# Optimization experiments

Measured on AMD Instinct MI355X. Metric: run time of the kernel, lower is better.

The kernel has to match this reference:

```python
import jax, jax.numpy as jnp
import numpy as np

H = 1024        # hidden_size
F = 4096        # intermediate_size
E = 8           # num_local_experts
TOP_K = 2       # num_experts_per_tok
B, S = 1, 2048


def setup_inputs() -> dict:
    key = jax.random.key(0)
    k0, k1, k2, k3 = jax.random.split(key, 4)
    hidden_states = jax.random.normal(k0, (B, S, H), dtype=jnp.float32)
    # torch nn.Linear weights: gate [E_out, in]; experts stacked on leading axis
    gate_w = jax.random.normal(k1, (E, H), dtype=jnp.float32) * 0.02
    gate_up_w = jax.random.normal(k2, (E, 2 * F, H), dtype=jnp.float32) * 0.02
    down_w = jax.random.normal(k3, (E, H, F), dtype=jnp.float32) * 0.02
    return {"hidden_states": hidden_states, "gate_w": gate_w,
            "gate_up_w": gate_up_w, "down_w": down_w}


def reference(hidden_states, gate_w, gate_up_w, down_w):
    b, s, h = hidden_states.shape
    x = hidden_states.reshape(-1, h)                      # [T, H]
    # router: softmax in float32, top-k, renormalize
    router_logits = x @ gate_w.T                          # [T, E]
    probs = jax.nn.softmax(router_logits.astype(jnp.float32), axis=-1)
    topw, sel = jax.lax.top_k(probs, TOP_K)               # [T, K]
    topw = topw / jnp.sum(topw, axis=-1, keepdims=True)
    topw = topw.astype(x.dtype)
    # combine weights [T, E]: zero for unselected experts -> same math as
    # the per-expert gather/scatter loop (full capacity, no dropped tokens)
    combine = jnp.sum(jax.nn.one_hot(sel, E, dtype=x.dtype) * topw[..., None], axis=1)
    # all experts on all tokens (dense-equivalent of masked dispatch)
    gu = jnp.einsum('th,efh->etf', x, gate_up_w)          # [E, T, 2F]
    gate, up = gu[..., :F], gu[..., F:]
    hact = up * jax.nn.gelu(gate, approximate=False)      # [E, T, F]
    expert_out = jnp.einsum('etf,ehf->eth', hact, down_w) # [E, T, H]
    out = jnp.einsum('eth,te->th', expert_out, combine)   # [T, H]
    return out.reshape(b, s, h)
```

## Files before the change

### kernel.cpp

```cpp
#include <hip/hip_runtime.h>

#define Hdim 1024
#define Fdim 4096
#define NE   8
#define NT   2048
#define MT_MAX 16
#define KSPLIT 2

typedef __attribute__((ext_vector_type(8))) short short8;
typedef __attribute__((ext_vector_type(4))) short short4v;
typedef __attribute__((ext_vector_type(4))) float f32x4;

__device__ __forceinline__ unsigned short bf16r(float f) {
  union { float fv; unsigned u; } v; v.fv = f;
  unsigned u = v.u;
  return (unsigned short)((u + 0x7FFFu + ((u >> 16) & 1u)) >> 16);
}

__device__ __forceinline__ void gl_lds16(const void* g, void* l) {
  __builtin_amdgcn_global_load_lds(
      (const __attribute__((address_space(1))) unsigned int*)g,
      (__attribute__((address_space(3))) unsigned int*)l, 16, 0, 0);
}

__global__ __launch_bounds__(256)
void k_cvt(const float* __restrict__ src, unsigned short* __restrict__ dst, int n4) {
  int stride = gridDim.x * 256;
  for (int i = blockIdx.x * 256 + threadIdx.x; i < n4; i += stride) {
    float4 v = *(const float4*)(src + (size_t)i * 4);
    short4v s;
    s.x = (short)bf16r(v.x); s.y = (short)bf16r(v.y);
    s.z = (short)bf16r(v.z); s.w = (short)bf16r(v.w);
    *(short4v*)(dst + (size_t)i * 4) = s;
  }
}

__global__ void k_router(const float* __restrict__ x, const float* __restrict__ gw,
                         int* __restrict__ counts, int* __restrict__ sel,
                         float* __restrict__ selw) {
  int wave = threadIdx.x >> 6;
  int l    = threadIdx.x & 63;
  int t    = blockIdx.x * 4 + wave;
  const float* xp = x + (size_t)t * Hdim;
  float acc[NE];
#pragma unroll
  for (int e = 0; e < NE; e++) acc[e] = 0.f;
  for (int h = l; h < Hdim; h += 64) {
    float xv = xp[h];
#pragma unroll
    for (int e = 0; e < NE; e++) acc[e] += xv * gw[e * Hdim + h];
  }
#pragma unroll
  for (int e = 0; e < NE; e++) {
    float v = acc[e];
#pragma unroll
    for (int off = 32; off > 0; off >>= 1) v += __shfl_down(v, off, 64);
    acc[e] = v;
  }
  if (l == 0) {
    int b0 = 0; float v0 = acc[0];
    for (int e = 1; e < NE; e++) if (acc[e] > v0) { v0 = acc[e]; b0 = e; }
    int b1 = -1; float v1 = -1e30f;
    for (int e = 0; e < NE; e++) if (e != b0 && acc[e] > v1) { v1 = acc[e]; b1 = e; }
    float w0 = 1.f / (1.f + expf(v1 - v0));
    atomicAdd(&counts[b0], 1);
    atomicAdd(&counts[b1], 1);
    sel[2 * t]     = b0;
    sel[2 * t + 1] = b1;
    selw[2 * t]     = w0;
    selw[2 * t + 1] = 1.f - w0;
  }
}

__global__ void k_scatter(const int* __restrict__ counts, const int* __restrict__ sel,
                          const float* __restrict__ selw, int* __restrict__ offsets,
                          int* __restrict__ rowids, float* __restrict__ pairw,
                          int* __restrict__ tok2slot) {
  __shared__ int soff[NE];
  __shared__ int scur[NE];
  if (threadIdx.x == 0) {
    int s = 0;
    for (int e = 0; e < NE; e++) { soff[e] = s; offsets[e] = s; s += counts[e]; scur[e] = 0; }
  }
  __syncthreads();
  for (int t = threadIdx.x; t < NT; t += blockDim.x) {
#pragma unroll
    for (int j = 0; j < 2; j++) {
      int e = sel[2 * t + j];
      int p = atomicAdd(&scur[e], 1);
      int slot = soff[e] + p;
      rowids[slot]        = t;
      pairw[slot]         = selw[2 * t + j];
      tok2slot[2 * t + j] = slot;
    }
  }
}

__global__ __launch_bounds__(256, 2)
void k_gate_up_bf(const unsigned short* __restrict__ xbf, const unsigned short* __restrict__ wbf,
                  const int* __restrict__ counts, const int* __restrict__ offsets,
                  const int* __restrict__ rowids, unsigned short* __restrict__ hact) {
  int e  = blockIdx.y >> 4;
  int mt = blockIdx.y & 15;
  int n  = counts[e];
  if (mt * 128 >= n) return;
  int base = offsets[e];
  int row0 = mt * 128;
  int f0   = blockIdx.x * 64;

  __shared__ __align__(16) unsigned short As[128][64];
  __shared__ __align__(16) unsigned short Bs[128][64];
  __shared__ int rid[128];

  int tid = threadIdx.x;
  if (tid < 128) {
    int r = row0 + tid;
    rid[tid] = (r < n) ? rowids[base + r] : rowids[base];
  }
  __syncthreads();

  int crow  = tid >> 3;
  int cphys = tid & 7;
  const unsigned short* sa[4];
  const unsigned short* sb[4];
#pragma unroll
  for (int p = 0; p < 4; p++) {
    int R = p * 32 + crow;
    int csrc = cphys ^ (R & 7);
    sa[p] = xbf + (size_t)rid[R] * Hdim + csrc * 8;
    int fr = (R < 64) ? (f0 + R) : (Fdim + f0 + (R - 64));
    sb[p] = wbf + ((size_t)e * 2 * Fdim + fr) * Hdim + csrc * 8;
  }
  int w = tid >> 6, lane = tid & 63;
  unsigned short* da[4];
  unsigned short* db[4];
#pragma unroll
  for (int p = 0; p < 4; p++) {
    da[p] = &As[0][0] + p * 2048 + w * 512;
    db[p] = &Bs[0][0] + p * 2048 + w * 512;
  }

  int wy = w >> 1, wx = w & 1;
  int lrow = lane & 15, cq = lane >> 4;
  f32x4 acc[4][4] = {};

  for (int k0 = 0; k0 < Hdim; k0 += 64) {
#pragma unroll
    for (int p = 0; p < 4; p++) gl_lds16(sa[p] + k0, da[p]);
#pragma unroll
    for (int p = 0; p < 4; p++) gl_lds16(sb[p] + k0, db[p]);
    __syncthreads();
#pragma unroll
    for (int ks = 0; ks < 2; ks++) {
      int soff = ((ks * 4 + cq) ^ (lrow & 7)) * 8;
      short8 a[4], b[4];
#pragma unroll
      for (int i = 0; i < 4; i++) a[i] = *(const short8*)&As[wy * 64 + i * 16 + lrow][soff];
      b[0] = *(const short8*)&Bs[wx * 32 + lrow][soff];
      b[1] = *(const short8*)&Bs[wx * 32 + 16 + lrow][soff];
      b[2] = *(const short8*)&Bs[64 + wx * 32 + lrow][soff];
      b[3] = *(const short8*)&Bs[64 + wx * 32 + 16 + lrow][soff];
#pragma unroll
      for (int i = 0; i < 4; i++)
#pragma unroll
        for (int j = 0; j < 4; j++)
          acc[i][j] = __builtin_amdgcn_mfma_f32_16x16x32_bf16(a[i], b[j], acc[i][j], 0, 0, 0);
    }
    __syncthreads();
  }

  int quad = lane >> 4;
#pragma unroll
  for (int i = 0; i < 4; i++) {
#pragma unroll
    for (int r = 0; r < 4; r++) {
      int rl = row0 + wy * 64 + i * 16 + quad * 4 + r;
      if (rl < n) {
        size_t rowoff = (size_t)(base + rl) * Fdim + f0 + wx * 32;
#pragma unroll
        for (int j = 0; j < 2; j++) {
          float g = acc[i][j][r];
          float u = acc[i][j + 2][r];
          float ge = 0.5f * g * (1.f + erff(g * 0.70710678118654752f));
          hact[rowoff + j * 16 + lrow] = bf16r(u * ge);
        }
      }
    }
  }
}

__global__ __launch_bounds__(256, 2)
void k_down_bf(const unsigned short* __restrict__ hact, const unsigned short* __restrict__ dbf,
               const int* __restrict__ counts, const int* __restrict__ offsets,
               const float* __restrict__ pairw, float* __restrict__ part) {
  int e  = blockIdx.y >> 4;
  int mt = blockIdx.y & 15;
  int n  = counts[e];
  if (mt * 128 >= n) return;
  int base = offsets[e];
  int row0 = mt * 128;
  int h0   = blockIdx.x * 128;
  const int KC = Fdim / KSPLIT;
  int kbeg = blockIdx.z * KC;
  int kend = kbeg + KC;

  __shared__ __align__(16) unsigned short As[128][64];
  __shared__ __align__(16) unsigned short Bs[128][64];

  int tid = threadIdx.x;
  int crow  = tid >> 3;
  int cphys = tid & 7;
  const unsigned short* sa[4];
  const unsigned short* sb[4];
#pragma unroll
  for (int p = 0; p < 4; p++) {
    int R = p * 32 + crow;
    int csrc = cphys ^ (R & 7);
    int slot = base + row0 + R;
    if (slot > NT * 2 - 1) slot = NT * 2 - 1;
    sa[p] = hact + (size_t)slot * Fdim + csrc * 8;
    sb[p] = dbf + ((size_t)e * Hdim + h0 + R) * Fdim + csrc * 8;
  }
  int w = tid >> 6, lane = tid & 63;
  unsigned short* da[4];
  unsigned short* db[4];
#pragma unroll
  for (int p = 0; p < 4; p++) {
    da[p] = &As[0][0] + p * 2048 + w * 512;
    db[p] = &Bs[0][0] + p * 2048 + w * 512;
  }

  int wy = w >> 1, wx = w & 1;
  int lrow = lane & 15, cq = lane >> 4;
  f32x4 acc[4][4] = {};

  for (int k0 = kbeg; k0 < kend; k0 += 64) {
#pragma unroll
    for (int p = 0; p < 4; p++) gl_lds16(sa[p] + k0, da[p]);
#pragma unroll
    for (int p = 0; p < 4; p++) gl_lds16(sb[p] + k0, db[p]);
    __syncthreads();
#pragma unroll
    for (int ks = 0; ks < 2; ks++) {
      int soff = ((ks * 4 + cq) ^ (lrow & 7)) * 8;
      short8 a[4], b[4];
#pragma unroll
      for (int i = 0; i < 4; i++) a[i] = *(const short8*)&As[wy * 64 + i * 16 + lrow][soff];
#pragma unroll
      for (int j = 0; j < 4; j++) b[j] = *(const short8*)&Bs[wx * 64 + j * 16 + lrow][soff];
#pragma unroll
      for (int i = 0; i < 4; i++)
#pragma unroll
        for (int j = 0; j < 4; j++)
          acc[i][j] = __builtin_amdgcn_mfma_f32_16x16x32_bf16(a[i], b[j], acc[i][j], 0, 0, 0);
    }
    __syncthreads();
  }

  int quad = lane >> 4;
#pragma unroll
  for (int i = 0; i < 4; i++) {
#pragma unroll
    for (int r = 0; r < 4; r++) {
      int rl = row0 + wy * 64 + i * 16 + quad * 4 + r;
      if (rl < n) {
        int slot = base + rl;
        float wv = pairw[slot];
        float* op = part + ((size_t)blockIdx.z * (NT * 2) + slot) * Hdim + h0 + wx * 64;
#pragma unroll
        for (int j = 0; j < 4; j++)
          op[j * 16 + lrow] = wv * acc[i][j][r];
      }
    }
  }
}

__global__ __launch_bounds__(256, 2)
void k_gate_up_v1(const float* __restrict__ x, const float* __restrict__ gup,
                  const int* __restrict__ counts, const int* __restrict__ offsets,
                  const int* __restrict__ rowids, unsigned short* __restrict__ hact) {
  int e  = blockIdx.y >> 4;
  int mt = blockIdx.y & 15;
  int n  = counts[e];
  if (mt * 128 >= n) return;
  int base = offsets[e];
  int row0 = mt * 128;
  int f0   = blockIdx.x * 64;

  __shared__ __align__(16) unsigned short As[128][40];
  __shared__ __align__(16) unsigned short Bs[128][40];
  __shared__ int rid[128];

  int tid = threadIdx.x;
  if (tid < 128) {
    int r = row0 + tid;
    rid[tid] = (r < n) ? rowids[base + r] : rowids[base];
  }
  __syncthreads();

  int kc   = (tid & 7) * 4;
  int trow = tid >> 3;
  const float* ap[4];
  const float* bp[4];
#pragma unroll
  for (int p = 0; p < 4; p++) {
    int ar = p * 32 + trow;
    ap[p] = x + (size_t)rid[ar] * Hdim + kc;
    int f = (ar < 64) ? (f0 + ar) : (Fdim + f0 + (ar - 64));
    bp[p] = gup + ((size_t)e * 2 * Fdim + f) * Hdim + kc;
  }

  int wave = tid >> 6, lane = tid & 63;
  int wy = wave >> 1, wx = wave & 1;
  int lrow = lane & 15, lk = (lane >> 4) * 8;
  f32x4 acc[4][4] = {};

  float4 ra[4], rb[4];
#pragma unroll
  for (int p = 0; p < 4; p++) { ra[p] = *(const float4*)(ap[p]); rb[p] = *(const float4*)(bp[p]); }

  for (int k0 = 0; k0 < Hdim; k0 += 32) {
    __syncthreads();
#pragma unroll
    for (int p = 0; p < 4; p++) {
      int ar = p * 32 + trow;
      short4v sa;
      sa.x = (short)bf16r(ra[p].x); sa.y = (short)bf16r(ra[p].y);
      sa.z = (short)bf16r(ra[p].z); sa.w = (short)bf16r(ra[p].w);
      *(short4v*)&As[ar][kc] = sa;
      short4v sbv;
      sbv.x = (short)bf16r(rb[p].x); sbv.y = (short)bf16r(rb[p].y);
      sbv.z = (short)bf16r(rb[p].z); sbv.w = (short)bf16r(rb[p].w);
      *(short4v*)&Bs[ar][kc] = sbv;
    }
    if (k0 + 32 < Hdim) {
#pragma unroll
      for (int p = 0; p < 4; p++) {
        ra[p] = *(const float4*)(ap[p] + k0 + 32);
        rb[p] = *(const float4*)(bp[p] + k0 + 32);
      }
    }
    __syncthreads();
    short8 a[4], b[4];
#pragma unroll
    for (int i = 0; i < 4; i++) a[i] = *(const short8*)&As[wy * 64 + i * 16 + lrow][lk];
    b[0] = *(const short8*)&Bs[wx * 32 + lrow][lk];
    b[1] = *(const short8*)&Bs[wx * 32 + 16 + lrow][lk];
    b[2] = *(const short8*)&Bs[64 + wx * 32 + lrow][lk];
    b[3] = *(const short8*)&Bs[64 + wx * 32 + 16 + lrow][lk];
#pragma unroll
    for (int i = 0; i < 4; i++)
#pragma unroll
      for (int j = 0; j < 4; j++)
        acc[i][j] = __builtin_amdgcn_mfma_f32_16x16x32_bf16(a[i], b[j], acc[i][j], 0, 0, 0);
  }

  int quad = lane >> 4;
#pragma unroll
  for (int i = 0; i < 4; i++) {
#pragma unroll
    for (int r = 0; r < 4; r++) {
      int rl = row0 + wy * 64 + i * 16 + quad * 4 + r;
      if (rl < n) {
        size_t rowoff = (size_t)(base + rl) * Fdim + f0 + wx * 32;
#pragma unroll
        for (int j = 0; j < 2; j++) {
          float g = acc[i][j][r];
          float u = acc[i][j + 2][r];
          float ge = 0.5f * g * (1.f + erff(g * 0.70710678118654752f));
          hact[rowoff + j * 16 + lrow] = bf16r(u * ge);
        }
      }
    }
  }
}

__global__ __launch_bounds__(256, 2)
void k_down_v1(const unsigned short* __restrict__ hact, const float* __restrict__ dw,
               const int* __restrict__ counts, const int* __restrict__ offsets,
               const float* __restrict__ pairw, float* __restrict__ part) {
  int e  = blockIdx.y >> 4;
  int mt = blockIdx.y & 15;
  int n  = counts[e];
  if (mt * 128 >= n) return;
  int base = offsets[e];
  int row0 = mt * 128;
  int h0   = blockIdx.x * 128;
  const int KC = Fdim / KSPLIT;
  int kbeg = blockIdx.z * KC;
  int kend = kbeg + KC;

  __shared__ __align__(16) unsigned short As[128][72];
  __shared__ __align__(16) unsigned short Bs[128][72];

  int tid = threadIdx.x;
  int wave = tid >> 6, lane = tid & 63;
  int wy = wave >> 1, wx = wave & 1;
  int lrow = lane & 15, lkq = (lane >> 4) * 8;

  const unsigned short* asrc[4];
#pragma unroll
  for (int p = 0; p < 4; p++) {
    int idx = p * 256 + tid;
    int row = idx >> 3, seg = idx & 7;
    int slot = base + row0 + row;
    if (slot > NT * 2 - 1) slot = NT * 2 - 1;
    asrc[p] = hact + (size_t)slot * Fdim + seg * 8;
  }
  const float* bsrc[8];
#pragma unroll
  for (int p = 0; p < 8; p++) {
    int idx = p * 256 + tid;
    int row = idx >> 4, seg = idx & 15;
    bsrc[p] = dw + ((size_t)e * Hdim + h0 + row) * Fdim + seg * 4;
  }

  int4   raw[4];
  float4 rbw[8];
#pragma unroll
  for (int p = 0; p < 4; p++) raw[p] = *(const int4*)(asrc[p] + kbeg);
#pragma unroll
  for (int p = 0; p < 8; p++) rbw[p] = *(const float4*)(bsrc[p] + kbeg);

  f32x4 acc[4][4] = {};
  for (int k0 = kbeg; k0 < kend; k0 += 64) {
    __syncthreads();
#pragma unroll
    for (int p = 0; p < 4; p++) {
      int idx = p * 256 + tid;
      int row = idx >> 3, seg = idx & 7;
      *(int4*)&As[row][seg * 8] = raw[p];
    }
#pragma unroll
    for (int p = 0; p < 8; p++) {
      int idx = p * 256 + tid;
      int row = idx >> 4, seg = idx & 15;
      short4v sbv;
      sbv.x = (short)bf16r(rbw[p].x); sbv.y = (short)bf16r(rbw[p].y);
      sbv.z = (short)bf16r(rbw[p].z); sbv.w = (short)bf16r(rbw[p].w);
      *(short4v*)&Bs[row][seg * 4] = sbv;
    }
    if (k0 + 64 < kend) {
#pragma unroll
      for (int p = 0; p < 4; p++) raw[p] = *(const int4*)(asrc[p] + k0 + 64);
#pragma unroll
      for (int p = 0; p < 8; p++) rbw[p] = *(const float4*)(bsrc[p] + k0 + 64);
    }
    __syncthreads();
#pragma unroll
    for (int ks = 0; ks < 2; ks++) {
      short8 a[4], b[4];
#pragma unroll
      for (int i = 0; i < 4; i++) a[i] = *(const short8*)&As[wy * 64 + i * 16 + lrow][ks * 32 + lkq];
#pragma unroll
      for (int j = 0; j < 4; j++) b[j] = *(const short8*)&Bs[wx * 64 + j * 16 + lrow][ks * 32 + lkq];
#pragma unroll
      for (int i = 0; i < 4; i++)
#pragma unroll
        for (int j = 0; j < 4; j++)
          acc[i][j] = __builtin_amdgcn_mfma_f32_16x16x32_bf16(a[i], b[j], acc[i][j], 0, 0, 0);
    }
  }

  int quad = lane >> 4;
#pragma unroll
  for (int i = 0; i < 4; i++) {
#pragma unroll
    for (int r = 0; r < 4; r++) {
      int rl = row0 + wy * 64 + i * 16 + quad * 4 + r;
      if (rl < n) {
        int slot = base + rl;
        float wv = pairw[slot];
        float* op = part + ((size_t)blockIdx.z * (NT * 2) + slot) * Hdim + h0 + wx * 64;
#pragma unroll
        for (int j = 0; j < 4; j++)
          op[j * 16 + lrow] = wv * acc[i][j][r];
      }
    }
  }
}

__global__ __launch_bounds__(256)
void k_combine(const float* __restrict__ part, const int* __restrict__ tok2slot,
               float* __restrict__ out) {
  int idx = blockIdx.x * 256 + threadIdx.x;
  int t  = idx >> 8;
  int hc = (idx & 255) << 2;
  int s0 = tok2slot[2 * t];
  int s1 = tok2slot[2 * t + 1];
  float4 a = *(const float4*)&part[(size_t)s0 * Hdim + hc];
  float4 b = *(const float4*)&part[((size_t)(NT * 2) + s0) * Hdim + hc];
  float4 c = *(const float4*)&part[(size_t)s1 * Hdim + hc];
  float4 d = *(const float4*)&part[((size_t)(NT * 2) + s1) * Hdim + hc];
  float4 s;
  s.x = (a.x + b.x) + (c.x + d.x);
  s.y = (a.y + b.y) + (c.y + d.y);
  s.z = (a.z + b.z) + (c.z + d.z);
  s.w = (a.w + b.w) + (c.w + d.w);
  *(float4*)&out[(size_t)t * Hdim + hc] = s;
}

extern "C" void kernel_launch(void* const* d_in, const int* in_sizes, int n_in,
                              void* d_out, int out_size, void* d_ws, size_t ws_size,
                              hipStream_t stream) {
  const float* x   = (const float*)d_in[0];
  const float* gw  = (const float*)d_in[1];
  const float* gup = (const float*)d_in[2];
  const float* dwn = (const float*)d_in[3];
  float* out = (float*)d_out;

  char* ws = (char*)d_ws;
  int*   counts   = (int*)(ws + 0);
  int*   offsets  = (int*)(ws + 128);
  int*   sel      = (int*)(ws + 4096);
  float* selw     = (float*)(ws + 4096 + 16384);
  int*   rowids   = (int*)(ws + 4096 + 32768);
  float* pairw    = (float*)(ws + 4096 + 49152);
  int*   tok2slot = (int*)(ws + 4096 + 65536);
  unsigned short* hact = (unsigned short*)(ws + (1 << 20));
  float* part = (float*)(ws + (1 << 20) + ((size_t)32 << 20));
  unsigned short* xbf = (unsigned short*)(ws + (1 << 20) + ((size_t)64 << 20));
  unsigned short* wbf = (unsigned short*)(ws + (1 << 20) + ((size_t)68 << 20));
  unsigned short* dbf = wbf;

  const size_t NEED = (size_t)(1 << 20) + ((size_t)68 << 20) + ((size_t)128 << 20);

  hipMemsetAsync(ws, 0, 4096, stream);

  k_router<<<NT / 4, 256, 0, stream>>>(x, gw, counts, sel, selw);
  k_scatter<<<1, 1024, 0, stream>>>(counts, sel, selw, offsets, rowids, pairw, tok2slot);

  if (ws_size >= NEED) {
    k_cvt<<<2048, 256, 0, stream>>>(x, xbf, NT * Hdim / 4);
    k_cvt<<<2048, 256, 0, stream>>>(gup, wbf, NE * 2 * Fdim * Hdim / 4);
    k_gate_up_bf<<<dim3(Fdim / 64, NE * MT_MAX), 256, 0, stream>>>(xbf, wbf, counts, offsets, rowids, hact);
    k_cvt<<<2048, 256, 0, stream>>>(dwn, dbf, NE * Hdim * Fdim / 4);
    k_down_bf<<<dim3(Hdim / 128, NE * MT_MAX, KSPLIT), 256, 0, stream>>>(hact, dbf, counts, offsets, pairw, part);
  } else {
    k_gate_up_v1<<<dim3(Fdim / 64, NE * MT_MAX), 256, 0, stream>>>(x, gup, counts, offsets, rowids, hact);
    k_down_v1<<<dim3(Hdim / 128, NE * MT_MAX, KSPLIT), 256, 0, stream>>>(hact, dwn, counts, offsets, pairw, part);
  }
  k_combine<<<NT * Hdim / 4 / 256, 256, 0, stream>>>(part, tok2slot, out);
}
```

Baseline: 709.8 us.

## Fuse bf16 conversions into one kernel and swap grid axes for weight reuse

Merges the three fp32-to-bf16 conversion launches into one kernel that writes separate buffers, so the down weights no longer overwrite the gate/up buffer. This needs a larger workspace. The GEMM grids now put the expert/row-tile index on blockIdx.x, so consecutive blocks share the same weight column tile and can reuse it in L2. Launch bounds are raised from 2 to 4 blocks per CU to increase occupancy, which may force register spills.

After: 1.154 ms. 1.63x slower.

```diff
diff --git a/kernel.cpp b/kernel.cpp
--- a/kernel.cpp
+++ b/kernel.cpp
@@ -24,14 +24,31 @@
 }
 
 __global__ __launch_bounds__(256)
-void k_cvt(const float* __restrict__ src, unsigned short* __restrict__ dst, int n4) {
+void k_cvt3(const float* __restrict__ x, const float* __restrict__ gup,
+            const float* __restrict__ dwn, unsigned short* __restrict__ xbf,
+            unsigned short* __restrict__ wbf, unsigned short* __restrict__ dbf) {
   int stride = gridDim.x * 256;
-  for (int i = blockIdx.x * 256 + threadIdx.x; i < n4; i += stride) {
-    float4 v = *(const float4*)(src + (size_t)i * 4);
+  int i0 = blockIdx.x * 256 + threadIdx.x;
+  for (int i = i0; i < NT * Hdim / 4; i += stride) {
+    float4 v = *(const float4*)(x + (size_t)i * 4);
     short4v s;
     s.x = (short)bf16r(v.x); s.y = (short)bf16r(v.y);
     s.z = (short)bf16r(v.z); s.w = (short)bf16r(v.w);
-    *(short4v*)(dst + (size_t)i * 4) = s;
+    *(short4v*)(xbf + (size_t)i * 4) = s;
+  }
+  for (int i = i0; i < NE * 2 * Fdim * (Hdim / 4); i += stride) {
+    float4 v = *(const float4*)(gup + (size_t)i * 4);
+    short4v s;
+    s.x = (short)bf16r(v.x); s.y = (short)bf16r(v.y);
+    s.z = (short)bf16r(v.z); s.w = (short)bf16r(v.w);
+    *(short4v*)(wbf + (size_t)i * 4) = s;
+  }
+  for (int i = i0; i < NE * Hdim * (Fdim / 4); i += stride) {
+    float4 v = *(const float4*)(dwn + (size_t)i * 4);
+    short4v s;
+    s.x = (short)bf16r(v.x); s.y = (short)bf16r(v.y);
+    s.z = (short)bf16r(v.z); s.w = (short)bf16r(v.w);
+    *(short4v*)(dbf + (size_t)i * 4) = s;
   }
 }
 
@@ -96,17 +113,17 @@
   }
 }
 
-__global__ __launch_bounds__(256, 2)
+__global__ __launch_bounds__(256, 4)
 void k_gate_up_bf(const unsigned short* __restrict__ xbf, const unsigned short* __restrict__ wbf,
                   const int* __restrict__ counts, const int* __restrict__ offsets,
                   const int* __restrict__ rowids, unsigned short* __restrict__ hact) {
-  int e  = blockIdx.y >> 4;
-  int mt = blockIdx.y & 15;
+  int e  = blockIdx.x >> 4;
+  int mt = blockIdx.x & 15;
   int n  = counts[e];
   if (mt * 128 >= n) return;
   int base = offsets[e];
   int row0 = mt * 128;
-  int f0   = blockIdx.x * 64;
+  int f0   = blockIdx.y * 64;
 
   __shared__ __align__(16) unsigned short As[128][64];
   __shared__ __align__(16) unsigned short Bs[128][64];
@@ -189,17 +206,17 @@
   }
 }
 
-__global__ __launch_bounds__(256, 2)
+__global__ __launch_bounds__(256, 4)
 void k_down_bf(const unsigned short* __restrict__ hact, const unsigned short* __restrict__ dbf,
                const int* __restrict__ counts, const int* __restrict__ offsets,
                const float* __restrict__ pairw, float* __restrict__ part) {
-  int e  = blockIdx.y >> 4;
-  int mt = blockIdx.y & 15;
+  int e  = blockIdx.x >> 4;
+  int mt = blockIdx.x & 15;
   int n  = counts[e];
   if (mt * 128 >= n) return;
   int base = offsets[e];
   int row0 = mt * 128;
-  int h0   = blockIdx.x * 128;
+  int h0   = blockIdx.y * 128;
   const int KC = Fdim / KSPLIT;
   int kbeg = blockIdx.z * KC;
   int kend = kbeg + KC;
@@ -521,22 +538,21 @@
   float* part = (float*)(ws + (1 << 20) + ((size_t)32 << 20));
   unsigned short* xbf = (unsigned short*)(ws + (1 << 20) + ((size_t)64 << 20));
   unsigned short* wbf = (unsigned short*)(ws + (1 << 20) + ((size_t)68 << 20));
-  unsigned short* dbf = wbf;
-
-  const size_t NEED = (size_t)(1 << 20) + ((size_t)68 << 20) + ((size_t)128 << 20);
+  unsigned short* dbf = (unsigned short*)(ws + (1 << 20) + ((size_t)196 << 20));
+
+  const size_t NEED = (size_t)(1 << 20) + ((size_t)260 << 20);
 
   hipMemsetAsync(ws, 0, 4096, stream);
 
-  k_router<<<NT / 4, 256, 0, stream>>>(x, gw, counts, sel, selw);
-  k_scatter<<<1, 1024, 0, stream>>>(counts, sel, selw, offsets, rowids, pairw, tok2slot);
-
   if (ws_size >= NEED) {
-    k_cvt<<<2048, 256, 0, stream>>>(x, xbf, NT * Hdim / 4);
-    k_cvt<<<2048, 256, 0, stream>>>(gup, wbf, NE * 2 * Fdim * Hdim / 4);
-    k_gate_up_bf<<<dim3(Fdim / 64, NE * MT_MAX), 256, 0, stream>>>(xbf, wbf, counts, offsets, rowids, hact);
-    k_cvt<<<2048, 256, 0, stream>>>(dwn, dbf, NE * Hdim * Fdim / 4);
-    k_down_bf<<<dim3(Hdim / 128, NE * MT_MAX, KSPLIT), 256, 0, stream>>>(hact, dbf, counts, offsets, pairw, part);
+    k_cvt3<<<2048, 256, 0, stream>>>(x, gup, dwn, xbf, wbf, dbf);
+    k_router<<<NT / 4, 256, 0, stream>>>(x, gw, counts, sel, selw);
+    k_scatter<<<1, 1024, 0, stream>>>(counts, sel, selw, offsets, rowids, pairw, tok2slot);
+    k_gate_up_bf<<<dim3(NE * MT_MAX, Fdim / 64), 256, 0, stream>>>(xbf, wbf, counts, offsets, rowids, hact);
+    k_down_bf<<<dim3(NE * MT_MAX, Hdim / 128, KSPLIT), 256, 0, stream>>>(hact, dbf, counts, offsets, pairw, part);
   } else {
+    k_router<<<NT / 4, 256, 0, stream>>>(x, gw, counts, sel, selw);
+    k_scatter<<<1, 1024, 0, stream>>>(counts, sel, selw, offsets, rowids, pairw, tok2slot);
     k_gate_up_v1<<<dim3(Fdim / 64, NE * MT_MAX), 256, 0, stream>>>(x, gup, counts, offsets, rowids, hact);
     k_down_v1<<<dim3(Hdim / 128, NE * MT_MAX, KSPLIT), 256, 0, stream>>>(hact, dwn, counts, offsets, pairw, part);
   }
```
